# Kernel optimization log

Measured on AMD Instinct MI355X. Metric: run time of the kernel, lower is better.

The kernel has to match this reference:

```python
import jax, jax.numpy as jnp
import numpy as np

HIDDEN = 2048
NUM_HEADS = 32
NUM_KV_HEADS = 8
HEAD_DIM = 128
EPS = 1e-6
ROPE_BASE = 10000.0
T = 2048


def setup_inputs() -> dict:
    key = jax.random.key(0)
    k1, k2, k3, k4, k5 = jax.random.split(key, 5)
    q_size = NUM_HEADS * HEAD_DIM
    kv_size = NUM_KV_HEADS * HEAD_DIM
    s = 0.02
    return {
        "positions": jnp.arange(T, dtype=jnp.int32),
        "hidden_states": jax.random.normal(k1, (T, HIDDEN), dtype=jnp.float32),
        "wqkv": jax.random.normal(k2, (q_size + 2 * kv_size, HIDDEN), dtype=jnp.float32) * s,
        "wo": jax.random.normal(k3, (HIDDEN, q_size), dtype=jnp.float32) * s,
        "q_norm_w": jnp.ones((HEAD_DIM,), dtype=jnp.float32),
        "k_norm_w": jnp.ones((HEAD_DIM,), dtype=jnp.float32),
    }


def _rms_norm(x, w, eps=EPS):
    # x: [T, H, D]; normalize over last dim
    var = jnp.mean(jnp.square(x), axis=-1, keepdims=True)
    return x * jax.lax.rsqrt(var + eps) * w


def _rope(positions, x):
    # neox-style rotate-half RoPE. x: [T, H, D]
    half = HEAD_DIM // 2
    inv_freq = 1.0 / (ROPE_BASE ** (jnp.arange(0, half, dtype=jnp.float32) / half))
    ang = positions.astype(jnp.float32)[:, None] * inv_freq  # [T, half]
    cos = jnp.cos(ang)[:, None, :]  # [T, 1, half]
    sin = jnp.sin(ang)[:, None, :]
    x1, x2 = x[..., :half], x[..., half:]
    return jnp.concatenate([x1 * cos - x2 * sin, x2 * cos + x1 * sin], axis=-1)


def reference(positions, hidden_states, wqkv, wo, q_norm_w, k_norm_w):
    q_size = NUM_HEADS * HEAD_DIM
    kv_size = NUM_KV_HEADS * HEAD_DIM
    scaling = HEAD_DIM ** -0.5

    qkv = hidden_states @ wqkv.T  # [T, q_size + 2*kv_size]
    q = qkv[:, :q_size].reshape(-1, NUM_HEADS, HEAD_DIM)
    k = qkv[:, q_size:q_size + kv_size].reshape(-1, NUM_KV_HEADS, HEAD_DIM)
    v = qkv[:, q_size + kv_size:].reshape(-1, NUM_KV_HEADS, HEAD_DIM)

    q = _rms_norm(q, q_norm_w)
    k = _rms_norm(k, k_norm_w)
    q = _rope(positions, q)
    k = _rope(positions, k)

    # GQA: repeat kv heads to match query heads
    group = NUM_HEADS // NUM_KV_HEADS
    k = jnp.repeat(k, group, axis=1)  # [T, H, D]
    v = jnp.repeat(v, group, axis=1)

    scores = jnp.einsum("thd,shd->hts", q, k) * scaling  # [H, T, T]
    causal = positions[:, None] >= positions[None, :]  # [T, T]
    scores = jnp.where(causal[None], scores, jnp.finfo(scores.dtype).min)
    probs = jax.nn.softmax(scores, axis=-1)
    o = jnp.einsum("hts,shd->thd", probs, v)  # [T, H, D]
    return o.reshape(-1, q_size) @ wo.T  # [T, HIDDEN]
```

## Files before the change

### kernel.cpp

```cpp
#include <hip/hip_runtime.h>
#include <hip/hip_bf16.h>

#define T_SEQ   2048
#define HIDDEN  2048
#define NUM_H   32
#define NUM_KV  8
#define HD      128
#define Q_SIZE  4096
#define QKV_N   6144

typedef __bf16 bf16;
typedef __bf16 bf16x8 __attribute__((ext_vector_type(8)));
typedef __bf16 bf16x4 __attribute__((ext_vector_type(4)));
typedef float  floatx4 __attribute__((ext_vector_type(4)));

#define GLOBAL_AS(p) ((const __attribute__((address_space(1))) void*)(p))
#define LDS_AS(p)    ((__attribute__((address_space(3))) void*)(p))

#define BARRIER() do { asm volatile("" ::: "memory"); \
                       __builtin_amdgcn_s_barrier();  \
                       asm volatile("" ::: "memory"); } while (0)
#define VMCNT(n) asm volatile("s_waitcnt vmcnt(" #n ")" ::: "memory")

__global__ void detect_dtype(const unsigned short* __restrict__ wq, int* flagp)
{
    const int lane = threadIdx.x;
    int cnt = 0;
    for (int i = lane; i < 512; i += 64) {
        int ef = (wq[i] >> 7) & 0xFF;
        if (ef >= 90 && ef <= 130) cnt++;
    }
    #pragma unroll
    for (int m = 32; m; m >>= 1) cnt += __shfl_xor(cnt, m);
    if (lane == 0) *flagp = (cnt >= 430) ? 1 : 0;
}

__global__ __launch_bounds__(256) void convert_all(
    const void* __restrict__ h, const void* __restrict__ wq,
    const void* __restrict__ wo_, const void* __restrict__ qn,
    const void* __restrict__ kn,
    bf16* __restrict__ hb, bf16* __restrict__ wqb, bf16* __restrict__ wob,
    bf16* __restrict__ qnb, bf16* __restrict__ knb, const int* flagp)
{
    long e = ((long)blockIdx.x * 256 + threadIdx.x) * 8;
    const void* src; bf16* dst; long off;
    if      (e < 4194304)  { src = h;   dst = hb;  off = e; }
    else if (e < 16777216) { src = wq;  dst = wqb; off = e - 4194304; }
    else if (e < 25165824) { src = wo_; dst = wob; off = e - 16777216; }
    else if (e < 25165952) { src = qn;  dst = qnb; off = e - 25165824; }
    else if (e < 25166080) { src = kn;  dst = knb; off = e - 25165952; }
    else return;

    if (*flagp) {
        *(bf16x8*)(dst + off) = *(const bf16x8*)((const bf16*)src + off);
    } else {
        const float* f = (const float*)src + off;
        bf16x8 v;
        #pragma unroll
        for (int i = 0; i < 8; ++i) v[i] = (bf16)f[i];
        *(bf16x8*)(dst + off) = v;
    }
}

__global__ __launch_bounds__(512, 2) void gemm8p(
    const bf16* __restrict__ A, const bf16* __restrict__ B,
    bf16* __restrict__ C, int N, int K, int lda, int ldb)
{
    __shared__ bf16 As[2][2][128 * 64];
    __shared__ bf16 Bs[2][192 * 64];

    const int tid  = threadIdx.x;
    const int wave = tid >> 6, lane = tid & 63;
    const int quad = lane >> 4, l16 = lane & 15;
    const int wm = wave >> 2;
    const int wn = wave & 3;
    const long baseN = (long)blockIdx.x * 192;
    const long baseM = (long)blockIdx.y * 256;

    const int sr  = tid >> 3;
    const int sgc = ((tid & 7) ^ (sr & 7)) * 8;

    auto stagePA = [&](int p, int g, int t) {
        const long kc = (long)t * 64;
        const bf16* src = A + (baseM + g * 64 + sr) * (long)lda + kc + sgc;
        __builtin_amdgcn_global_load_lds(GLOBAL_AS(src),
            LDS_AS(&As[p][0][g * 4096 + wave * 512]), 16, 0, 0);
        __builtin_amdgcn_global_load_lds(GLOBAL_AS(src + 128 * (long)lda),
            LDS_AS(&As[p][1][g * 4096 + wave * 512]), 16, 0, 0);
    };
    auto stagePBu = [&](int p, int u, int t) {
        const long kc = (long)t * 64;
        const bf16* src = B + (baseN + u * 64 + sr) * (long)ldb + kc + sgc;
        __builtin_amdgcn_global_load_lds(GLOBAL_AS(src),
            LDS_AS(&Bs[p][u * 4096 + wave * 512]), 16, 0, 0);
    };

    floatx4 acc[8][3] = {};
    bf16x8 af[4][2], bf01[2][2], bf2[2];

    auto rdAf = [&](int p, int g) {
        #pragma unroll
        for (int mf = 0; mf < 4; ++mf)
            #pragma unroll
            for (int ks = 0; ks < 2; ++ks) {
                const int r = g * 64 + mf * 16 + l16;
                af[mf][ks] = *(const bf16x8*)(&As[p][wm][r * 64 + (((ks * 4 + quad) ^ (r & 7)) * 8)]);
            }
    };
    auto rdB01 = [&](int p) {
        #pragma unroll
        for (int nf = 0; nf < 2; ++nf)
            #pragma unroll
            for (int ks = 0; ks < 2; ++ks) {
                const int r = wn * 48 + nf * 16 + l16;
                bf01[nf][ks] = *(const bf16x8*)(&Bs[p][r * 64 + (((ks * 4 + quad) ^ (r & 7)) * 8)]);
            }
    };
    auto rdB2 = [&](int p) {
        #pragma unroll
        for (int ks = 0; ks < 2; ++ks) {
            const int r = wn * 48 + 32 + l16;
            bf2[ks] = *(const bf16x8*)(&Bs[p][r * 64 + (((ks * 4 + quad) ^ (r & 7)) * 8)]);
        }
    };
    auto mmQ2 = [&](int mo) {
        __builtin_amdgcn_s_setprio(1);
        #pragma unroll
        for (int mf = 0; mf < 4; ++mf)
            #pragma unroll
            for (int nf = 0; nf < 2; ++nf)
                #pragma unroll
                for (int ks = 0; ks < 2; ++ks)
                    acc[mo + mf][nf] = __builtin_amdgcn_mfma_f32_16x16x32_bf16(
                        af[mf][ks], bf01[nf][ks], acc[mo + mf][nf], 0, 0, 0);
        __builtin_amdgcn_s_setprio(0);
    };
    auto mmQ1 = [&](int mo) {
        __builtin_amdgcn_s_setprio(1);
        #pragma unroll
        for (int mf = 0; mf < 4; ++mf)
            #pragma unroll
            for (int ks = 0; ks < 2; ++ks)
                acc[mo + mf][2] = __builtin_amdgcn_mfma_f32_16x16x32_bf16(
                    af[mf][ks], bf2[ks], acc[mo + mf][2], 0, 0, 0);
        __builtin_amdgcn_s_setprio(0);
    };

    stagePBu(0, 0, 0); stagePBu(0, 1, 0); stagePBu(0, 2, 0);
    stagePA(0, 0, 0);  stagePA(0, 1, 0);
    stagePBu(1, 0, 1);
    VMCNT(1);
    BARRIER();

    const int NT2 = K / 128;
    for (int j = 0; j < NT2; ++j) {
        const int t1 = 2 * j + 1;
        const bool more = (j + 1 < NT2);

        rdAf(0, 0); rdB01(0);
        stagePBu(1, 1, t1); stagePBu(1, 2, t1);
        BARRIER(); __builtin_amdgcn_sched_barrier(0);
        mmQ2(0);
        BARRIER();
        rdB2(0);
        stagePA(1, 0, t1);
        VMCNT(5);
        BARRIER(); __builtin_amdgcn_sched_barrier(0);
        mmQ1(0);
        BARRIER();
        rdAf(0, 1);
        stagePA(1, 1, t1);
        BARRIER(); __builtin_amdgcn_sched_barrier(0);
        mmQ2(4);
        BARRIER();
        if (more) { stagePBu(0, 0, t1 + 1); VMCNT(3); } else { VMCNT(2); }
        BARRIER(); __builtin_amdgcn_sched_barrier(0);
        mmQ1(4);
        BARRIER();
        rdAf(1, 0); rdB01(1);
        if (more) { stagePBu(0, 1, t1 + 1); stagePBu(0, 2, t1 + 1); }
        BARRIER(); __builtin_amdgcn_sched_barrier(0);
        mmQ2(0);
        BARRIER();
        rdB2(1);
        if (more) { stagePA(0, 0, t1 + 1); VMCNT(5); } else { VMCNT(0); }
        BARRIER(); __builtin_amdgcn_sched_barrier(0);
        mmQ1(0);
        BARRIER();
        rdAf(1, 1);
        if (more) stagePA(0, 1, t1 + 1);
        BARRIER(); __builtin_amdgcn_sched_barrier(0);
        mmQ2(4);
        BARRIER();
        if (more) { stagePBu(1, 0, t1 + 2); VMCNT(3); }
        BARRIER(); __builtin_amdgcn_sched_barrier(0);
        mmQ1(4);
        BARRIER();
    }

    #pragma unroll
    for (int i = 0; i < 8; ++i)
        #pragma unroll
        for (int j = 0; j < 3; ++j)
            #pragma unroll
            for (int r = 0; r < 4; ++r) {
                long row = baseM + wm * 128 + i * 16 + quad * 4 + r;
                long col = baseN + wn * 48 + j * 16 + l16;
                C[row * (long)N + col] = (bf16)acc[i][j][r];
            }
}

__global__ __launch_bounds__(256) void gemm_db(
    const bf16* __restrict__ A, const bf16* __restrict__ B,
    float* __restrict__ Cp, int N, int Kd, int lda, int ldb)
{
    __shared__ bf16 As[2][128 * 32];
    __shared__ bf16 Bs[2][128 * 32];

    const int tid  = threadIdx.x;
    const int wave = tid >> 6, lane = tid & 63;
    const int quad = lane >> 4, l16 = lane & 15;
    const int wm = (wave & 1) * 64, wn = (wave >> 1) * 64;
    const long baseM = (long)blockIdx.x * 128;
    const long baseN = (long)blockIdx.y * 128;
    const long koff  = (long)blockIdx.z * Kd;

    const int  srow = wave * 16 + (lane >> 2);
    const int  scol = (lane & 3) * 8;
    const long aoff0 = (baseM + srow) * (long)lda + koff + scol;
    const long aoff1 = (baseM + 64 + srow) * (long)lda + koff + scol;
    const long boff0 = (baseN + srow) * (long)ldb + koff + scol;
    const long boff1 = (baseN + 64 + srow) * (long)ldb + koff + scol;
    const int  lds0 = wave * 512;
    const int  lds1 = 2048 + wave * 512;

    auto stage = [&](int p, int k0) {
        __builtin_amdgcn_global_load_lds(GLOBAL_AS(A + aoff0 + k0), LDS_AS(As[p] + lds0), 16, 0, 0);
        __builtin_amdgcn_global_load_lds(GLOBAL_AS(A + aoff1 + k0), LDS_AS(As[p] + lds1), 16, 0, 0);
        __builtin_amdgcn_global_load_lds(GLOBAL_AS(B + boff0 + k0), LDS_AS(Bs[p] + lds0), 16, 0, 0);
        __builtin_amdgcn_global_load_lds(GLOBAL_AS(B + boff1 + k0), LDS_AS(Bs[p] + lds1), 16, 0, 0);
    };

    floatx4 acc[4][4] = {};

    stage(0, 0);
    asm volatile("s_waitcnt vmcnt(0)" ::: "memory");
    __builtin_amdgcn_s_barrier();

    int cur = 0;
    for (int k0 = 0; k0 < Kd; k0 += 32) {
        if (k0 + 32 < Kd) stage(cur ^ 1, k0 + 32);
        __builtin_amdgcn_sched_barrier(0);

        bf16x8 af[4], bfr[4];
        #pragma unroll
        for (int i = 0; i < 4; ++i)
            af[i] = *(const bf16x8*)(As[cur] + (wm + i * 16 + l16) * 32 + quad * 8);
        #pragma unroll
        for (int j = 0; j < 4; ++j)
            bfr[j] = *(const bf16x8*)(Bs[cur] + (wn + j * 16 + l16) * 32 + quad * 8);

        #pragma unroll
        for (int i = 0; i < 4; ++i)
            #pragma unroll
            for (int j = 0; j < 4; ++j)
                acc[i][j] = __builtin_amdgcn_mfma_f32_16x16x32_bf16(af[i], bfr[j], acc[i][j], 0, 0, 0);

        asm volatile("s_waitcnt vmcnt(0)" ::: "memory");
        __builtin_amdgcn_s_barrier();
        cur ^= 1;
    }

    const long Mrows = (long)gridDim.x * 128;
    float* C = Cp + (long)blockIdx.z * Mrows * N;
    #pragma unroll
    for (int i = 0; i < 4; ++i)
        #pragma unroll
        for (int j = 0; j < 4; ++j)
            #pragma unroll
            for (int r = 0; r < 4; ++r) {
                long row = baseM + wm + i * 16 + quad * 4 + r;
                long col = baseN + wn + j * 16 + l16;
                C[row * (long)N + col] = acc[i][j][r];
            }
}

__global__ __launch_bounds__(256) void reduce2(
    const float* __restrict__ P0, const float* __restrict__ P1,
    void* __restrict__ out, const int* flagp)
{
    long i = ((long)blockIdx.x * 256 + threadIdx.x) * 4;
    floatx4 a = *(const floatx4*)(P0 + i);
    floatx4 b = *(const floatx4*)(P1 + i);
    floatx4 s = a + b;
    if (*flagp) {
        bf16x4 o;
        #pragma unroll
        for (int r = 0; r < 4; ++r) o[r] = (bf16)s[r];
        *(bf16x4*)((bf16*)out + i) = o;
    } else {
        *(floatx4*)((float*)out + i) = s;
    }
}

__global__ __launch_bounds__(256) void qkv_post(
    bf16* __restrict__ qkv, const int* __restrict__ positions,
    const bf16* __restrict__ qnw, const bf16* __restrict__ knw)
{
    const int t = blockIdx.x;
    const int tid = threadIdx.x, wave = tid >> 6, lane = tid & 63;
    const float pos = (float)positions[t];

    const float inv = expf(-(float)lane * (float)(9.210340371976184 / 64.0));
    float sn, cs;
    sincosf(pos * inv, &sn, &cs);

    bf16* row = qkv + (long)t * QKV_N;

    for (int u = wave; u < 40; u += 4) {
        bf16* p       = (u < 32) ? row + u * HD : row + Q_SIZE + (u - 32) * HD;
        const bf16* w = (u < 32) ? qnw : knw;
        float x1 = (float)p[lane], x2 = (float)p[lane + 64];
        float ss = x1 * x1 + x2 * x2;
        #pragma unroll
        for (int m = 32; m; m >>= 1) ss += __shfl_xor(ss, m);
        float rr = rsqrtf(ss * (1.f / 128.f) + 1e-6f);
        float y1 = x1 * rr * (float)w[lane];
        float y2 = x2 * rr * (float)w[lane + 64];
        p[lane]      = (bf16)(y1 * cs - y2 * sn);
        p[lane + 64] = (bf16)(y2 * cs + y1 * sn);
    }
}

__global__ __launch_bounds__(256) void vtrans(const bf16* __restrict__ qkv,
                                              bf16* __restrict__ vt)
{
    __shared__ bf16 tile[64][136];
    const int t0 = blockIdx.x * 64, kvh = blockIdx.y, tid = threadIdx.x;

    const int rl = tid >> 4, c8 = (tid & 15) * 8;
    const bf16* src = qkv + (long)t0 * QKV_N + 5120 + kvh * HD;
    #pragma unroll
    for (int it = 0; it < 4; ++it) {
        int r = it * 16 + rl;
        *(bf16x8*)(&tile[r][c8]) = *(const bf16x8*)(src + (long)r * QKV_N + c8);
    }
    __syncthreads();

    const int d = tid >> 1, tb = (tid & 1) * 32;
    bf16* dst = vt + ((long)kvh * HD + d) * T_SEQ + t0 + tb;
    #pragma unroll
    for (int it = 0; it < 4; ++it) {
        bf16x8 v;
        #pragma unroll
        for (int j = 0; j < 8; ++j) v[j] = tile[tb + it * 8 + j][d];
        *(bf16x8*)(dst + it * 8) = v;
    }
}

__global__ __launch_bounds__(256, 3) void attn5(bf16* qkv, const bf16* __restrict__ vt)
{
    __shared__ bf16 Ks[2][64 * 128];
    __shared__ bf16 Vs[128 * 64];

    const int tid  = threadIdx.x, wave = tid >> 6, lane = tid & 63;
    const int quad = lane >> 4, l16 = lane & 15;
    const int h = blockIdx.x, kvh = h >> 2;
    const int iq = 31 - blockIdx.y;
    const int q0 = iq * 64;

    const float C1 = 0.12753236f;
    const float C2 = 17.312340f;

    bf16x8 qf[4];
    {
        const bf16* qa = qkv + (long)(q0 + wave * 16 + l16) * QKV_N + h * HD + quad * 8;
        #pragma unroll
        for (int ks = 0; ks < 4; ++ks) qf[ks] = *(const bf16x8*)(qa + ks * 32);
    }

    floatx4 oacc[8] = {};
    float ls = 0.f;

    const int krl = lane >> 4, kc = lane & 15;
    const int vrl = lane >> 3, vc = lane & 7;
    const int kswz = (kc ^ (wave * 4 + krl)) * 8;
    const int vswz = (vc ^ (vrl & 7)) * 8;
    const int wsig = ((wave & 1) << 1) | (wave >> 1);
    const int sq4  = (((quad & 1) << 1) | (quad >> 1)) << 2;

    const bf16* kg0 = qkv + Q_SIZE + kvh * HD;
    const bf16* vg0 = vt + (long)kvh * HD * T_SEQ;

    auto stageK = [&](int p, int kt) {
        const bf16* kg = kg0 + (long)(kt * 64) * QKV_N;
        #pragma unroll
        for (int it = 0; it < 4; ++it) {
            const int rK = it * 16 + wsig * 4 + krl;
            __builtin_amdgcn_global_load_lds(GLOBAL_AS(kg + (long)rK * QKV_N + kswz),
                                             LDS_AS(&Ks[p][it * 2048 + wave * 512]), 16, 0, 0);
        }
    };
    auto stageV = [&](int kt) {
        const bf16* vg = vg0 + kt * 64;
        #pragma unroll
        for (int it = 0; it < 4; ++it) {
            const int dV = it * 32 + wave * 8 + vrl;
            __builtin_amdgcn_global_load_lds(GLOBAL_AS(vg + (long)dV * T_SEQ + vswz),
                                             LDS_AS(&Vs[it * 2048 + wave * 512]), 16, 0, 0);
        }
    };

    stageK(0, 0);

    const int qg = q0 + wave * 16 + l16;

    for (int kt = 0; kt <= iq; ++kt) {
        const int p = kt & 1;
        __syncthreads();
        stageV(kt);
        if (kt < iq) stageK(p ^ 1, kt + 1);

        const int k0 = kt * 64;

        floatx4 sT[4] = {};
        #pragma unroll
        for (int j2 = 0; j2 < 4; ++j2)
            #pragma unroll
            for (int ks = 0; ks < 4; ++ks) {
                bf16x8 kf = *(const bf16x8*)(&Ks[p][(j2 * 16 + l16) * 128 + (((ks * 4 + quad) ^ l16) * 8)]);
                sT[j2] = __builtin_amdgcn_mfma_f32_16x16x32_bf16(kf, qf[ks], sT[j2], 0, 0, 0);
            }

        const bool diag = (kt == iq);
        unsigned lov[4], hiv[4];
        #pragma unroll
        for (int j2 = 0; j2 < 4; ++j2) {
            float ev[4];
            #pragma unroll
            for (int r = 0; r < 4; ++r) {
                float x = __builtin_amdgcn_exp2f(sT[j2][r] * C1 - C2);
                if (diag && (k0 + j2 * 16 + sq4 + r > qg)) x = 0.f;
                ls += x;
                ev[r] = x;
            }
            asm("v_cvt_pk_bf16_f32 %0, %1, %2" : "=v"(lov[j2]) : "v"(ev[0]), "v"(ev[1]));
            asm("v_cvt_pk_bf16_f32 %0, %1, %2" : "=v"(hiv[j2]) : "v"(ev[2]), "v"(ev[3]));
        }

        bf16x8 pa[2];
        #pragma unroll
        for (int ks2 = 0; ks2 < 2; ++ks2) {
            auto wl = __builtin_amdgcn_permlane32_swap(lov[2 * ks2], lov[2 * ks2 + 1], false, false);
            auto wh = __builtin_amdgcn_permlane32_swap(hiv[2 * ks2], hiv[2 * ks2 + 1], false, false);
            union { unsigned w[4]; bf16x8 v; } u;
            u.w[0] = wl[0]; u.w[1] = wh[0]; u.w[2] = wl[1]; u.w[3] = wh[1];
            pa[ks2] = u.v;
        }

        if (kt < iq) asm volatile("s_waitcnt vmcnt(4)" ::: "memory");
        else         asm volatile("s_waitcnt vmcnt(0)" ::: "memory");
        __builtin_amdgcn_s_barrier();
        __builtin_amdgcn_sched_barrier(0);

        #pragma unroll
        for (int ks2 = 0; ks2 < 2; ++ks2)
            #pragma unroll
            for (int vj = 0; vj < 8; ++vj) {
                const int d = vj * 16 + l16;
                bf16x8 vb = *(const bf16x8*)(&Vs[d * 64 + (((ks2 * 4 + quad) ^ (d & 7)) * 8)]);
                oacc[vj] = __builtin_amdgcn_mfma_f32_16x16x32_bf16(pa[ks2], vb, oacc[vj], 0, 0, 0);
            }
    }

    ls += __shfl_xor(ls, 16); ls += __shfl_xor(ls, 32);
    float rinv[4];
    #pragma unroll
    for (int r = 0; r < 4; ++r) rinv[r] = 1.f / __shfl(ls, quad * 4 + r);

    #pragma unroll
    for (int vj = 0; vj < 8; ++vj)
        #pragma unroll
        for (int r = 0; r < 4; ++r) {
            const long row = q0 + wave * 16 + quad * 4 + r;
            qkv[row * (long)QKV_N + h * HD + vj * 16 + l16] = (bf16)(oacc[vj][r] * rinv[r]);
        }
}

extern "C" void kernel_launch(void* const* d_in, const int* in_sizes, int n_in,
                              void* d_out, int out_size, void* d_ws, size_t ws_size,
                              hipStream_t stream)
{
    const int* positions = (const int*)d_in[0];

    char* ws = (char*)d_ws;
    bf16* qkv  = (bf16*)(ws);
    bf16* hb   = (bf16*)(ws + 25165824);
    bf16* vt   = hb;
    float* P0  = (float*)(ws + 25165824);
    float* P1  = (float*)(ws + 41943040);
    bf16* wqb  = (bf16*)(ws + 33554432);
    bf16* wob  = (bf16*)(ws + 58720256);
    bf16* qnb  = (bf16*)(ws + 75497472);
    bf16* knb  = (bf16*)(ws + 75497728);
    int*  flag = (int*) (ws + 75497984);

    detect_dtype<<<dim3(1), dim3(64), 0, stream>>>((const unsigned short*)d_in[2], flag);
    convert_all<<<dim3(12289), dim3(256), 0, stream>>>(
        d_in[1], d_in[2], d_in[3], d_in[4], d_in[5],
        hb, wqb, wob, qnb, knb, flag);

    gemm8p<<<dim3(QKV_N / 192, T_SEQ / 256), dim3(512), 0, stream>>>(
        hb, wqb, qkv, QKV_N, HIDDEN, HIDDEN, HIDDEN);
    vtrans<<<dim3(T_SEQ / 64, NUM_KV), dim3(256), 0, stream>>>(qkv, vt);
    qkv_post<<<dim3(T_SEQ), dim3(256), 0, stream>>>(qkv, positions, qnb, knb);
    attn5<<<dim3(NUM_H, 32), dim3(256), 0, stream>>>(qkv, vt);
    gemm_db<<<dim3(T_SEQ / 128, HIDDEN / 128, 2), dim3(256), 0, stream>>>(
        qkv, wob, P0, HIDDEN, Q_SIZE / 2, QKV_N, Q_SIZE);
    reduce2<<<dim3(4096), dim3(256), 0, stream>>>(P0, P1, d_out, flag);
}
```

Before: 319.0 us.

## Double K-tile to 64 with XOR-swizzled LDS in output projection GEMM

The output-projection split-K GEMM now stages 64-wide K tiles instead of 32, with an XOR swizzle on LDS column chunks to avoid bank conflicts. It waits only on the older loads (vmcnt 8) so the next tile's prefetch overlaps compute, and it raises wave priority around the MFMA block. This is meant to halve the barrier and wait overhead per K step and improve LDS read efficiency. LDS use doubles to 64KB per block, which may limit occupancy despite the launch_bounds hint of 2 blocks.

```diff
diff --git a/kernel.cpp b/kernel.cpp
--- a/kernel.cpp
+++ b/kernel.cpp
@@ -162,36 +162,43 @@
         BARRIER(); __builtin_amdgcn_sched_barrier(0);
         mmQ2(0);
         BARRIER();
+
         rdB2(0);
         stagePA(1, 0, t1);
         VMCNT(5);
         BARRIER(); __builtin_amdgcn_sched_barrier(0);
         mmQ1(0);
         BARRIER();
+
         rdAf(0, 1);
         stagePA(1, 1, t1);
         BARRIER(); __builtin_amdgcn_sched_barrier(0);
         mmQ2(4);
         BARRIER();
+
         if (more) { stagePBu(0, 0, t1 + 1); VMCNT(3); } else { VMCNT(2); }
         BARRIER(); __builtin_amdgcn_sched_barrier(0);
         mmQ1(4);
         BARRIER();
+
         rdAf(1, 0); rdB01(1);
         if (more) { stagePBu(0, 1, t1 + 1); stagePBu(0, 2, t1 + 1); }
         BARRIER(); __builtin_amdgcn_sched_barrier(0);
         mmQ2(0);
         BARRIER();
+
         rdB2(1);
         if (more) { stagePA(0, 0, t1 + 1); VMCNT(5); } else { VMCNT(0); }
         BARRIER(); __builtin_amdgcn_sched_barrier(0);
         mmQ1(0);
         BARRIER();
+
         rdAf(1, 1);
         if (more) stagePA(0, 1, t1 + 1);
         BARRIER(); __builtin_amdgcn_sched_barrier(0);
         mmQ2(4);
         BARRIER();
+
         if (more) { stagePBu(1, 0, t1 + 2); VMCNT(3); }
         BARRIER(); __builtin_amdgcn_sched_barrier(0);
         mmQ1(4);
@@ -210,12 +217,12 @@
             }
 }
 
-__global__ __launch_bounds__(256) void gemm_db(
+__global__ __launch_bounds__(256, 2) void gemm_db64(
     const bf16* __restrict__ A, const bf16* __restrict__ B,
     float* __restrict__ Cp, int N, int Kd, int lda, int ldb)
 {
-    __shared__ bf16 As[2][128 * 32];
-    __shared__ bf16 Bs[2][128 * 32];
+    __shared__ bf16 As[2][128 * 64];
+    __shared__ bf16 Bs[2][128 * 64];
 
     const int tid  = threadIdx.x;
     const int wave = tid >> 6, lane = tid & 63;
@@ -225,49 +232,64 @@
     const long baseN = (long)blockIdx.y * 128;
     const long koff  = (long)blockIdx.z * Kd;
 
-    const int  srow = wave * 16 + (lane >> 2);
-    const int  scol = (lane & 3) * 8;
-    const long aoff0 = (baseM + srow) * (long)lda + koff + scol;
-    const long aoff1 = (baseM + 64 + srow) * (long)lda + koff + scol;
-    const long boff0 = (baseN + srow) * (long)ldb + koff + scol;
-    const long boff1 = (baseN + 64 + srow) * (long)ldb + koff + scol;
-    const int  lds0 = wave * 512;
-    const int  lds1 = 2048 + wave * 512;
-
-    auto stage = [&](int p, int k0) {
-        __builtin_amdgcn_global_load_lds(GLOBAL_AS(A + aoff0 + k0), LDS_AS(As[p] + lds0), 16, 0, 0);
-        __builtin_amdgcn_global_load_lds(GLOBAL_AS(A + aoff1 + k0), LDS_AS(As[p] + lds1), 16, 0, 0);
-        __builtin_amdgcn_global_load_lds(GLOBAL_AS(B + boff0 + k0), LDS_AS(Bs[p] + lds0), 16, 0, 0);
-        __builtin_amdgcn_global_load_lds(GLOBAL_AS(B + boff1 + k0), LDS_AS(Bs[p] + lds1), 16, 0, 0);
+    const int sr  = tid >> 3;
+    const int sgc = ((tid & 7) ^ (sr & 7)) * 8;
+
+    auto stage = [&](int p, int t) {
+        const long kc = koff + (long)t * 64;
+        #pragma unroll
+        for (int u = 0; u < 4; ++u) {
+            const bf16* sa = A + (baseM + u * 32 + sr) * (long)lda + kc + sgc;
+            __builtin_amdgcn_global_load_lds(GLOBAL_AS(sa),
+                LDS_AS(&As[p][u * 2048 + wave * 512]), 16, 0, 0);
+        }
+        #pragma unroll
+        for (int u = 0; u < 4; ++u) {
+            const bf16* sb = B + (baseN + u * 32 + sr) * (long)ldb + kc + sgc;
+            __builtin_amdgcn_global_load_lds(GLOBAL_AS(sb),
+                LDS_AS(&Bs[p][u * 2048 + wave * 512]), 16, 0, 0);
+        }
     };
 
     floatx4 acc[4][4] = {};
 
     stage(0, 0);
-    asm volatile("s_waitcnt vmcnt(0)" ::: "memory");
-    __builtin_amdgcn_s_barrier();
-
+
+    const int NT = Kd / 64;
     int cur = 0;
-    for (int k0 = 0; k0 < Kd; k0 += 32) {
-        if (k0 + 32 < Kd) stage(cur ^ 1, k0 + 32);
-        __builtin_amdgcn_sched_barrier(0);
-
-        bf16x8 af[4], bfr[4];
+    for (int t = 0; t < NT; ++t) {
+        if (t + 1 < NT) { stage(cur ^ 1, t + 1); VMCNT(8); }
+        else            { VMCNT(0); }
+        BARRIER();
+
+        bf16x8 af[4][2], bfr[4][2];
         #pragma unroll
         for (int i = 0; i < 4; ++i)
-            af[i] = *(const bf16x8*)(As[cur] + (wm + i * 16 + l16) * 32 + quad * 8);
+            #pragma unroll
+            for (int ks = 0; ks < 2; ++ks) {
+                const int r = wm + i * 16 + l16;
+                af[i][ks] = *(const bf16x8*)(&As[cur][r * 64 + (((ks * 4 + quad) ^ (r & 7)) * 8)]);
+            }
         #pragma unroll
         for (int j = 0; j < 4; ++j)
-            bfr[j] = *(const bf16x8*)(Bs[cur] + (wn + j * 16 + l16) * 32 + quad * 8);
-
+            #pragma unroll
+            for (int ks = 0; ks < 2; ++ks) {
+                const int r = wn + j * 16 + l16;
+                bfr[j][ks] = *(const bf16x8*)(&Bs[cur][r * 64 + (((ks * 4 + quad) ^ (r & 7)) * 8)]);
+            }
+
+        __builtin_amdgcn_s_setprio(1);
         #pragma unroll
         for (int i = 0; i < 4; ++i)
             #pragma unroll
             for (int j = 0; j < 4; ++j)
-                acc[i][j] = __builtin_amdgcn_mfma_f32_16x16x32_bf16(af[i], bfr[j], acc[i][j], 0, 0, 0);
-
-        asm volatile("s_waitcnt vmcnt(0)" ::: "memory");
-        __builtin_amdgcn_s_barrier();
+                #pragma unroll
+                for (int ks = 0; ks < 2; ++ks)
+                    acc[i][j] = __builtin_amdgcn_mfma_f32_16x16x32_bf16(
+                        af[i][ks], bfr[j][ks], acc[i][j], 0, 0, 0);
+        __builtin_amdgcn_s_setprio(0);
+
+        BARRIER();
         cur ^= 1;
     }
 
@@ -515,7 +537,7 @@
     vtrans<<<dim3(T_SEQ / 64, NUM_KV), dim3(256), 0, stream>>>(qkv, vt);
     qkv_post<<<dim3(T_SEQ), dim3(256), 0, stream>>>(qkv, positions, qnb, knb);
     attn5<<<dim3(NUM_H, 32), dim3(256), 0, stream>>>(qkv, vt);
-    gemm_db<<<dim3(T_SEQ / 128, HIDDEN / 128, 2), dim3(256), 0, stream>>>(
+    gemm_db64<<<dim3(T_SEQ / 128, HIDDEN / 128, 2), dim3(256), 0, stream>>>(
         qkv, wob, P0, HIDDEN, Q_SIZE / 2, QKV_N, Q_SIZE);
     reduce2<<<dim3(4096), dim3(256), 0, stream>>>(P0, P1, d_out, flag);
 }
```

New measurement: 308.2 us. 1.04x faster.
